# Optimization experiments

Hardware: AMD Instinct MI355X
Metric: run time of the kernel (lower is better)

## Reference

```python
import jax, jax.numpy as jnp
import numpy as np

B, S, E, H = 4, 2048, 1024, 16
HD = E // H  # head_dim = 64
EPS = 1.1920928955078125e-07  # torch.finfo(float32).eps (RMSNorm eps=None default)


def _rmsnorm(x, w):
    # normalize over last dim
    ms = jnp.mean(x * x, axis=-1, keepdims=True)
    return x * jax.lax.rsqrt(ms + EPS) * w


def _rope(x, start_pos=0):
    # x: [B, H, S, HD]; interleaved (even/odd) rotary embedding
    seq_len = x.shape[-2]
    inv_freq = 1.0 / (10000.0 ** (jnp.arange(0, HD, 2, dtype=jnp.float32) / HD))  # [HD/2]
    t = jnp.arange(start_pos, start_pos + seq_len, dtype=jnp.float32)  # [S]
    freqs = t[:, None] * inv_freq[None, :]  # [S, HD/2]
    cos = jnp.cos(freqs)[None, None]  # [1,1,S,HD/2]
    sin = jnp.sin(freqs)[None, None]
    x1 = x[..., 0::2]
    x2 = x[..., 1::2]
    o1 = x1 * cos - x2 * sin
    o2 = x1 * sin + x2 * cos
    # stack(..., -1).flatten(-2) -> re-interleave
    return jnp.stack((o1, o2), axis=-1).reshape(x.shape)


def setup_inputs() -> dict:
    key = jax.random.key(0)
    k1, k2, k3, k4 = jax.random.split(key, 4)
    lim = 1.0 / np.sqrt(E)
    return {
        "q": jax.random.normal(k1, (B, S, E), jnp.float32),
        "k": jax.random.normal(k2, (B, S, E), jnp.float32),
        "v": jax.random.normal(k3, (B, S, E), jnp.float32),
        "q_norm_w": jnp.ones((HD,), jnp.float32),
        "k_norm_w": jnp.ones((HD,), jnp.float32),
        "proj_w": jax.random.uniform(k4, (E, E), jnp.float32, -lim, lim),
        "proj_b": jnp.zeros((E,), jnp.float32),
    }


def reference(q, k, v, q_norm_w, k_norm_w, proj_w, proj_b):
    b, s, _ = q.shape
    scale = HD ** -0.5
    # [B,S,E] -> [B,H,S,HD]
    qh = q.reshape(b, s, H, HD).transpose(0, 2, 1, 3)
    kh = k.reshape(b, s, H, HD).transpose(0, 2, 1, 3)
    vh = v.reshape(b, s, H, HD).transpose(0, 2, 1, 3)
    # per-head QK RMSNorm then RoPE
    qh = _rope(_rmsnorm(qh, q_norm_w))
    kh = _rope(_rmsnorm(kh, k_norm_w))
    # explicit attention (no mask path)
    scores = jnp.einsum("bhqd,bhkd->bhqk", qh, kh) * scale  # [B,H,S,S]
    attn = jax.nn.softmax(scores, axis=-1)
    ctx = jnp.einsum("bhqk,bhkd->bhqd", attn, vh)
    ctx = ctx.transpose(0, 2, 1, 3).reshape(b, s, E)
    return ctx @ proj_w.T + proj_b
```

## Files before the change

### kernel.cpp

```cpp
#include <hip/hip_runtime.h>
#include <hip/hip_bf16.h>
#include <cstdint>

#define B_ 4
#define S_ 2048
#define E_ 1024
#define H_ 16
#define HD_ 64
#define EPS_ 1.1920928955078125e-07f

typedef __attribute__((ext_vector_type(8))) short shortx8;
typedef __attribute__((ext_vector_type(4))) float floatx4;
typedef __attribute__((ext_vector_type(8))) _Float16 halfx8;
typedef __attribute__((ext_vector_type(2))) __fp16 fp16x2;

#define C1_ 0.18033688068389154f

__global__ __launch_bounds__(256) void prep(
    const float* __restrict__ q, const float* __restrict__ k,
    const float* __restrict__ v,
    const float* __restrict__ qw, const float* __restrict__ kw,
    const float* __restrict__ pw,
    __hip_bfloat16* __restrict__ qh, __hip_bfloat16* __restrict__ kh,
    _Float16* __restrict__ vt, __hip_bfloat16* __restrict__ wb)
{
    __shared__ _Float16 tile[64][72];
    const int bid = blockIdx.x;
    const int tid = threadIdx.x;

    if (bid < 16384) {
        const size_t PT = (size_t)B_ * S_ * E_ / 4;
        size_t t = (size_t)bid * 256 + tid;
        const bool is_k = (t >= PT);
        if (is_k) t -= PT;

        const int row = (int)(t >> 8);
        const int b   = row / S_;
        const int s   = row % S_;
        const int grp = (int)(t & 255);
        const int h   = grp >> 4;
        const int dl  = (grp & 15) * 4;

        const float* __restrict__ src = is_k ? k : q;
        const float* __restrict__ w   = is_k ? kw : qw;
        __hip_bfloat16* __restrict__ dst = is_k ? kh : qh;

        const float4 x  = ((const float4*)src)[t];
        const float4 wv = ((const float4*)w)[grp & 15];

        float ss = x.x * x.x + x.y * x.y + x.z * x.z + x.w * x.w;
#pragma unroll
        for (int m = 1; m < 16; m <<= 1) ss += __shfl_xor(ss, m);
        float r = rsqrtf(ss * (1.0f / HD_) + EPS_);
        if (!is_k) r *= C1_;

        const float xn0 = x.x * r * wv.x;
        const float xn1 = x.y * r * wv.y;
        const float xn2 = x.z * r * wv.z;
        const float xn3 = x.w * r * wv.w;

        const float L2I = 0.41524101186092029f;
        const int   i0  = dl >> 1;
        const float f0  = (float)s * __builtin_amdgcn_exp2f(-(float)i0 * L2I);
        const float f1  = (float)s * __builtin_amdgcn_exp2f(-(float)(i0 + 1) * L2I);
        const float c0 = __cosf(f0), sn0 = __sinf(f0);
        const float c1 = __cosf(f1), sn1 = __sinf(f1);

        __hip_bfloat16 pk[4];
        pk[0] = __float2bfloat16(xn0 * c0 - xn1 * sn0);
        pk[1] = __float2bfloat16(xn0 * sn0 + xn1 * c0);
        pk[2] = __float2bfloat16(xn2 * c1 - xn3 * sn1);
        pk[3] = __float2bfloat16(xn2 * sn1 + xn3 * c1);
        *(ushort4*)(dst + ((size_t)((b * H_ + h) * S_ + s)) * HD_ + dl) =
            *(const ushort4*)pk;
    } else if (bid < 18432) {
        const int bb2 = bid - 16384;
        const int s0  = (bb2 & 31) * 64;
        const int bh  = bb2 >> 5;
        const int b   = bh >> 4, h = bh & 15;
        {
            const int sl = tid >> 2;
            const int o  = sl;
            const int n  = (o & 32) | (((o >> 2) & 3) << 3) |
                           (((o >> 4) & 1) << 2) | (o & 3);
            const int d0 = (tid & 3) * 16;
            const float* __restrict__ src =
                v + ((size_t)(b * S_ + s0 + sl)) * E_ + h * HD_ + d0;
            float4 f0 = ((const float4*)src)[0];
            float4 f1 = ((const float4*)src)[1];
            float4 f2 = ((const float4*)src)[2];
            float4 f3 = ((const float4*)src)[3];
            float vals[16] = {f0.x,f0.y,f0.z,f0.w, f1.x,f1.y,f1.z,f1.w,
                              f2.x,f2.y,f2.z,f2.w, f3.x,f3.y,f3.z,f3.w};
#pragma unroll
            for (int j = 0; j < 16; ++j)
                tile[d0 + j][n] = (_Float16)vals[j];
        }
        __syncthreads();
        {
            const int d  = tid >> 2;
            const int sg = (tid & 3) * 16;
            _Float16* __restrict__ dst =
                vt + ((size_t)(bh * HD_ + d)) * S_ + s0 + sg;
            ((uint4*)dst)[0] = *(const uint4*)&tile[d][sg];
            ((uint4*)dst)[1] = *(const uint4*)&tile[d][sg + 8];
        }
    } else {
        const int i = (bid - 18432) * 256 + tid;
        float4 f = ((const float4*)pw)[i];
        wb[4 * i + 0] = __float2bfloat16(f.x);
        wb[4 * i + 1] = __float2bfloat16(f.y);
        wb[4 * i + 2] = __float2bfloat16(f.z);
        wb[4 * i + 3] = __float2bfloat16(f.w);
    }
}

__global__ __launch_bounds__(256, 4) void attn(
    const __hip_bfloat16* __restrict__ qh, const __hip_bfloat16* __restrict__ kh,
    const _Float16* __restrict__ vt, __hip_bfloat16* __restrict__ ctx)
{
    __shared__ __hip_bfloat16 Kt[128][72];
    __shared__ _Float16       Vt[64][152];

    const int bid  = blockIdx.x;
    const int slot = bid >> 3;
    const int bh   = ((bid & 7) << 3) | (slot & 7);
    const int q0   = (slot >> 3) * 128;
    const int tid  = threadIdx.x;
    const int wv   = tid >> 6;
    const int lane = tid & 63;
    const int l16  = lane & 15;
    const int quad = lane >> 4;
    const int b    = bh >> 4, h = bh & 15;

    shortx8 aq[2][2];
#pragma unroll
    for (int mh = 0; mh < 2; ++mh) {
        const __hip_bfloat16* qbase =
            qh + ((size_t)bh * S_ + q0 + wv * 32 + mh * 16 + l16) * HD_;
        aq[mh][0] = *(const shortx8*)(qbase + quad * 8);
        aq[mh][1] = *(const shortx8*)(qbase + 32 + quad * 8);
    }

    const halfx8 ones = {(_Float16)1.f, (_Float16)1.f, (_Float16)1.f, (_Float16)1.f,
                         (_Float16)1.f, (_Float16)1.f, (_Float16)1.f, (_Float16)1.f};

    floatx4 O[2][4] = {};
    floatx4 O5[2]   = {};

    const __hip_bfloat16* __restrict__ kbase = kh + (size_t)bh * S_ * HD_;
    const _Float16* __restrict__ vbase = vt + (size_t)bh * HD_ * S_;

    const int sr = tid >> 1, sc = (tid & 1) * 32;
    const int vr = tid >> 2, vc = (tid & 3) * 32;

    for (int kt = 0; kt < S_ / 128; ++kt) {
        {
            const uint4* kp = (const uint4*)(kbase +
                (size_t)(kt * 128 + sr) * HD_ + sc);
            uint4 k0 = kp[0], k1 = kp[1], k2 = kp[2], k3 = kp[3];
            *(uint4*)&Kt[sr][sc]      = k0;
            *(uint4*)&Kt[sr][sc + 8]  = k1;
            *(uint4*)&Kt[sr][sc + 16] = k2;
            *(uint4*)&Kt[sr][sc + 24] = k3;
        }
        {
            const uint4* vp = (const uint4*)(vbase +
                (size_t)vr * S_ + kt * 128 + vc);
            uint4 v0 = vp[0], v1 = vp[1], v2 = vp[2], v3 = vp[3];
            *(uint4*)&Vt[vr][vc]      = v0;
            *(uint4*)&Vt[vr][vc + 8]  = v1;
            *(uint4*)&Vt[vr][vc + 16] = v2;
            *(uint4*)&Vt[vr][vc + 24] = v3;
        }
        __syncthreads();

#pragma unroll
        for (int hk = 0; hk < 2; ++hk) {
            halfx8 bb[2][2];
#pragma unroll
            for (int f = 0; f < 2; ++f) {
                floatx4 s4p[2][2];
                __builtin_amdgcn_s_setprio(1);
#pragma unroll
                for (int nt2 = 0; nt2 < 2; ++nt2) {
                    const int nt = 2 * f + nt2;
                    const shortx8 kb0 =
                        *(const shortx8*)&Kt[hk * 64 + nt * 16 + l16][quad * 8];
                    const shortx8 kb1 =
                        *(const shortx8*)&Kt[hk * 64 + nt * 16 + l16][32 + quad * 8];
#pragma unroll
                    for (int mh = 0; mh < 2; ++mh) {
                        floatx4 c = {0.f, 0.f, 0.f, 0.f};
                        c = __builtin_amdgcn_mfma_f32_16x16x32_bf16(kb0, aq[mh][0], c, 0, 0, 0);
                        c = __builtin_amdgcn_mfma_f32_16x16x32_bf16(kb1, aq[mh][1], c, 0, 0, 0);
                        s4p[mh][nt2] = c;
                    }
                }
                __builtin_amdgcn_s_setprio(0);
#pragma unroll
                for (int mh = 0; mh < 2; ++mh) {
                    union { fp16x2 h2[4]; halfx8 h8; } u;
                    u.h2[0] = __builtin_amdgcn_cvt_pkrtz(
                        __builtin_amdgcn_exp2f(s4p[mh][0][0]),
                        __builtin_amdgcn_exp2f(s4p[mh][0][1]));
                    u.h2[1] = __builtin_amdgcn_cvt_pkrtz(
                        __builtin_amdgcn_exp2f(s4p[mh][0][2]),
                        __builtin_amdgcn_exp2f(s4p[mh][0][3]));
                    u.h2[2] = __builtin_amdgcn_cvt_pkrtz(
                        __builtin_amdgcn_exp2f(s4p[mh][1][0]),
                        __builtin_amdgcn_exp2f(s4p[mh][1][1]));
                    u.h2[3] = __builtin_amdgcn_cvt_pkrtz(
                        __builtin_amdgcn_exp2f(s4p[mh][1][2]),
                        __builtin_amdgcn_exp2f(s4p[mh][1][3]));
                    bb[mh][f] = u.h8;
                }
            }

            __builtin_amdgcn_s_setprio(1);
#pragma unroll
            for (int mh = 0; mh < 2; ++mh) {
                O5[mh] = __builtin_amdgcn_mfma_f32_16x16x32_f16(ones, bb[mh][0], O5[mh], 0, 0, 0);
                O5[mh] = __builtin_amdgcn_mfma_f32_16x16x32_f16(ones, bb[mh][1], O5[mh], 0, 0, 0);
            }

#pragma unroll
            for (int dt = 0; dt < 4; ++dt) {
                const _Float16* vrow = &Vt[dt * 16 + l16][hk * 64];
                const halfx8 A0 = *(const halfx8*)(vrow + quad * 8);
                const halfx8 A1 = *(const halfx8*)(vrow + 32 + quad * 8);
#pragma unroll
                for (int mh = 0; mh < 2; ++mh) {
                    O[mh][dt] = __builtin_amdgcn_mfma_f32_16x16x32_f16(
                        A0, bb[mh][0], O[mh][dt], 0, 0, 0);
                    O[mh][dt] = __builtin_amdgcn_mfma_f32_16x16x32_f16(
                        A1, bb[mh][1], O[mh][dt], 0, 0, 0);
                }
            }
            __builtin_amdgcn_s_setprio(0);
        }
        __syncthreads();
    }

#pragma unroll
    for (int mh = 0; mh < 2; ++mh) {
        const float inv = 1.0f / O5[mh][0];
        const int s = q0 + wv * 32 + mh * 16 + l16;
        __hip_bfloat16* cb = ctx + ((size_t)(b * S_ + s)) * E_ + h * HD_;
#pragma unroll
        for (int dt = 0; dt < 4; ++dt) {
            __hip_bfloat16 pk[4];
#pragma unroll
            for (int r = 0; r < 4; ++r)
                pk[r] = __float2bfloat16(O[mh][dt][r] * inv);
            *(ushort4*)(cb + dt * 16 + quad * 4) = *(const ushort4*)pk;
        }
    }
}

__global__ __launch_bounds__(256) void proj(
    const __hip_bfloat16* __restrict__ ctx, const __hip_bfloat16* __restrict__ wb,
    const float* __restrict__ bias, float* __restrict__ out)
{
    __shared__ __hip_bfloat16 As[128][64];
    __shared__ __hip_bfloat16 Bs[128][64];

    const int bid  = blockIdx.x;
    const int slot = bid >> 3;
    const int mblk = ((bid & 7) << 3) | (slot & 7);
    const int nblk = slot >> 3;
    const int m0 = mblk * 128;
    const int n0 = nblk * 128;
    const int tid  = threadIdx.x;
    const int wv   = tid >> 6;
    const int lane = tid & 63;
    const int l16  = lane & 15;
    const int quad = lane >> 4;
    const int wr   = (wv >> 1) * 64;
    const int wc   = (wv & 1) * 64;

    const int crow = lane >> 3;
    const int ccol = (lane & 7) * 8;

    floatx4 acc[4][4] = {};

    for (int k0 = 0; k0 < E_; k0 += 64) {
#pragma unroll
        for (int j = 0; j < 4; ++j) {
            const int r8 = (wv * 4 + j) * 8;
            const __hip_bfloat16* ga =
                ctx + (size_t)(m0 + r8 + crow) * E_ + k0 + ccol;
            const __hip_bfloat16* gb =
                wb  + (size_t)(n0 + r8 + crow) * E_ + k0 + ccol;
            __builtin_amdgcn_global_load_lds(
                (const __attribute__((address_space(1))) void*)ga,
                (__attribute__((address_space(3))) void*)((char*)&As[0][0] + r8 * 128),
                16, 0, 0);
            __builtin_amdgcn_global_load_lds(
                (const __attribute__((address_space(1))) void*)gb,
                (__attribute__((address_space(3))) void*)((char*)&Bs[0][0] + r8 * 128),
                16, 0, 0);
        }
        __syncthreads();

#pragma unroll
        for (int ks = 0; ks < 2; ++ks) {
            shortx8 af[4], bf4[4];
#pragma unroll
            for (int mt = 0; mt < 4; ++mt)
                af[mt] = *(const shortx8*)&As[wr + mt * 16 + l16][ks * 32 + quad * 8];
#pragma unroll
            for (int nt = 0; nt < 4; ++nt)
                bf4[nt] = *(const shortx8*)&Bs[wc + nt * 16 + l16][ks * 32 + quad * 8];

#pragma unroll
            for (int mt = 0; mt < 4; ++mt)
#pragma unroll
                for (int nt = 0; nt < 4; ++nt)
                    acc[mt][nt] = __builtin_amdgcn_mfma_f32_16x16x32_bf16(
                        af[mt], bf4[nt], acc[mt][nt], 0, 0, 0);
        }
        __syncthreads();
    }

#pragma unroll
    for (int nt = 0; nt < 4; ++nt) {
        const float bv = bias[n0 + wc + nt * 16 + l16];
#pragma unroll
        for (int mt = 0; mt < 4; ++mt)
#pragma unroll
            for (int r = 0; r < 4; ++r) {
                const int mrow = m0 + wr + mt * 16 + quad * 4 + r;
                const int ncol = n0 + wc + nt * 16 + l16;
                out[(size_t)mrow * E_ + ncol] = acc[mt][nt][r] + bv;
            }
    }
}

extern "C" void kernel_launch(void* const* d_in, const int* in_sizes, int n_in,
                              void* d_out, int out_size, void* d_ws, size_t ws_size,
                              hipStream_t stream)
{
    const float* q  = (const float*)d_in[0];
    const float* k  = (const float*)d_in[1];
    const float* v  = (const float*)d_in[2];
    const float* qw = (const float*)d_in[3];
    const float* kw = (const float*)d_in[4];
    const float* pw = (const float*)d_in[5];
    const float* pb = (const float*)d_in[6];
    float* out = (float*)d_out;

    char* ws = (char*)d_ws;
    const size_t SEG = (size_t)B_ * H_ * S_ * HD_ * 2;
    __hip_bfloat16* qh  = (__hip_bfloat16*)(ws);
    __hip_bfloat16* kh  = (__hip_bfloat16*)(ws + SEG);
    _Float16*       vt  = (_Float16*)(ws + 2 * SEG);
    __hip_bfloat16* ctx = (__hip_bfloat16*)(ws + 3 * SEG);
    __hip_bfloat16* wbp = (__hip_bfloat16*)(ws + 4 * SEG);

    prep<<<dim3(19456), 256, 0, stream>>>(q, k, v, qw, kw, pw, qh, kh, vt, wbp);
    attn<<<dim3(1024), 256, 0, stream>>>(qh, kh, vt, ctx);
    proj<<<dim3(512), 256, 0, stream>>>(ctx, wbp, pb, out);
}
```

Measured before the change: 248.4 us.

## Load K/V tiles with direct global-to-LDS loads and XOR-swizzled layout

Replaces the register-staged global->LDS copy of K and V tiles with global_load_lds, which writes 16 bytes per lane straight into shared memory. Padding is removed, and an XOR swizzle on the global source addresses and the LDS read addresses avoids bank conflicts. This cuts VGPR staging and the separate LDS store instructions. The risk is that the swizzle mapping must exactly match the 16-byte-per-lane placement, and the loads are still not double-buffered.

```diff
diff --git a/kernel.cpp b/kernel.cpp
--- a/kernel.cpp
+++ b/kernel.cpp
@@ -119,8 +119,8 @@
     const __hip_bfloat16* __restrict__ qh, const __hip_bfloat16* __restrict__ kh,
     const _Float16* __restrict__ vt, __hip_bfloat16* __restrict__ ctx)
 {
-    __shared__ __hip_bfloat16 Kt[128][72];
-    __shared__ _Float16       Vt[64][152];
+    __shared__ __hip_bfloat16 Kt[128][64];
+    __shared__ _Float16       Vt[64][128];
 
     const int bid  = blockIdx.x;
     const int slot = bid >> 3;
@@ -148,30 +148,38 @@
     floatx4 O[2][4] = {};
     floatx4 O5[2]   = {};
 
-    const __hip_bfloat16* __restrict__ kbase = kh + (size_t)bh * S_ * HD_;
-    const _Float16* __restrict__ vbase = vt + (size_t)bh * HD_ * S_;
-
-    const int sr = tid >> 1, sc = (tid & 1) * 32;
-    const int vr = tid >> 2, vc = (tid & 3) * 32;
+    const char* __restrict__ kbase = (const char*)(kh + (size_t)bh * S_ * HD_);
+    const char* __restrict__ vbase = (const char*)(vt + (size_t)bh * HD_ * S_);
+
+    int koff[4], voff[4];
+#pragma unroll
+    for (int j = 0; j < 4; ++j) {
+        const int krow = wv * 32 + j * 8 + (lane >> 3);
+        koff[j] = krow * 128 + (((lane & 7) * 16) ^ ((krow & 7) << 4));
+        const int vrow = wv * 16 + j * 4 + (lane >> 4);
+        voff[j] = vrow * (S_ * 2) + (((lane & 15) * 16) ^ ((vrow & 15) << 4));
+    }
+
+    const int kswz = (l16 & 7) << 4;
+    const int kc0  = (quad * 16) ^ kswz;
+    const int kc1  = (64 + quad * 16) ^ kswz;
+    const int vswz = l16 << 4;
 
     for (int kt = 0; kt < S_ / 128; ++kt) {
-        {
-            const uint4* kp = (const uint4*)(kbase +
-                (size_t)(kt * 128 + sr) * HD_ + sc);
-            uint4 k0 = kp[0], k1 = kp[1], k2 = kp[2], k3 = kp[3];
-            *(uint4*)&Kt[sr][sc]      = k0;
-            *(uint4*)&Kt[sr][sc + 8]  = k1;
-            *(uint4*)&Kt[sr][sc + 16] = k2;
-            *(uint4*)&Kt[sr][sc + 24] = k3;
-        }
-        {
-            const uint4* vp = (const uint4*)(vbase +
-                (size_t)vr * S_ + kt * 128 + vc);
-            uint4 v0 = vp[0], v1 = vp[1], v2 = vp[2], v3 = vp[3];
-            *(uint4*)&Vt[vr][vc]      = v0;
-            *(uint4*)&Vt[vr][vc + 8]  = v1;
-            *(uint4*)&Vt[vr][vc + 16] = v2;
-            *(uint4*)&Vt[vr][vc + 24] = v3;
+#pragma unroll
+        for (int j = 0; j < 4; ++j) {
+            __builtin_amdgcn_global_load_lds(
+                (const __attribute__((address_space(1))) void*)
+                    (kbase + (size_t)kt * 16384 + koff[j]),
+                (__attribute__((address_space(3))) void*)
+                    ((char*)&Kt[0][0] + (wv * 32 + j * 8) * 128),
+                16, 0, 0);
+            __builtin_amdgcn_global_load_lds(
+                (const __attribute__((address_space(1))) void*)
+                    (vbase + (size_t)kt * 256 + voff[j]),
+                (__attribute__((address_space(3))) void*)
+                    ((char*)&Vt[0][0] + (wv * 16 + j * 4) * 256),
+                16, 0, 0);
         }
         __syncthreads();
 
@@ -185,10 +193,10 @@
 #pragma unroll
                 for (int nt2 = 0; nt2 < 2; ++nt2) {
                     const int nt = 2 * f + nt2;
-                    const shortx8 kb0 =
-                        *(const shortx8*)&Kt[hk * 64 + nt * 16 + l16][quad * 8];
-                    const shortx8 kb1 =
-                        *(const shortx8*)&Kt[hk * 64 + nt * 16 + l16][32 + quad * 8];
+                    const char* kr =
+                        (const char*)&Kt[0][0] + (hk * 64 + nt * 16 + l16) * 128;
+                    const shortx8 kb0 = *(const shortx8*)(kr + kc0);
+                    const shortx8 kb1 = *(const shortx8*)(kr + kc1);
 #pragma unroll
                     for (int mh = 0; mh < 2; ++mh) {
                         floatx4 c = {0.f, 0.f, 0.f, 0.f};
@@ -226,9 +234,11 @@
 
 #pragma unroll
             for (int dt = 0; dt < 4; ++dt) {
-                const _Float16* vrow = &Vt[dt * 16 + l16][hk * 64];
-                const halfx8 A0 = *(const halfx8*)(vrow + quad * 8);
-                const halfx8 A1 = *(const halfx8*)(vrow + 32 + quad * 8);
+                const char* vr = (const char*)&Vt[0][0] + (dt * 16 + l16) * 256;
+                const halfx8 A0 =
+                    *(const halfx8*)(vr + ((hk * 128 + quad * 16) ^ vswz));
+                const halfx8 A1 =
+                    *(const halfx8*)(vr + ((hk * 128 + 64 + quad * 16) ^ vswz));
 #pragma unroll
                 for (int mh = 0; mh < 2; ++mh) {
                     O[mh][dt] = __builtin_amdgcn_mfma_f32_16x16x32_f16(
```

Measured after the change: 248.1 us. Within noise of the previous version (-0.1%).
